# Performance work log

Hardware: AMD Instinct MI355X
Metric: run time of the kernel (lower is better)

## Reference

```python
import jax, jax.numpy as jnp
import numpy as np

DIM = 512
K = 64          # num_clusters
GHOST = 1
ALPHA = 100.0
EPS = 1e-12


def _l2norm(v, axis):
    return v / jnp.maximum(jnp.linalg.norm(v, axis=axis, keepdims=True), EPS)


def setup_inputs() -> dict:
    key = jax.random.key(0)
    k_x, k_c = jax.random.split(key)
    x = jax.random.normal(k_x, (64, DIM, 32, 32), dtype=jnp.float32)
    # centroids ~ orthogonal init in torch; random normal rows, unit-ish scale
    centroids = jax.random.normal(k_c, (K + GHOST, DIM), dtype=jnp.float32) / np.sqrt(DIM)
    conv_w = 2.0 * ALPHA * centroids            # [K+g, C] (1x1 conv kernel squeezed)
    conv_b = -ALPHA * jnp.linalg.norm(centroids, axis=1)  # [K+g]
    return {"x": x, "centroids": centroids, "conv_w": conv_w, "conv_b": conv_b}


def reference(x, centroids, conv_w, conv_b):
    N, C, H, W = x.shape
    L = H * W
    # descriptor-wise L2 normalization over channel dim
    xn = _l2norm(x, axis=1)
    xf = xn.reshape(N, C, L)                                   # [N, C, L]
    # 1x1 conv == per-location matmul; softmax over clusters
    logits = jnp.einsum('kc,ncl->nkl', conv_w, xf) + conv_b[None, :, None]
    a = jax.nn.softmax(logits, axis=1)                         # [N, K+g, L]
    # vlad[n,k,c] = sum_l a[n,k,l]*(x[n,c,l]-cent[k,c])
    #            = (a @ x^T) - (sum_l a) * cent   -- avoids NxKxCxL tensor
    weighted = jnp.einsum('nkl,ncl->nkc', a, xf)               # [N, K+g, C]
    a_sum = jnp.sum(a, axis=-1)                                # [N, K+g]
    vlad = weighted - a_sum[:, :, None] * centroids[None]      # [N, K+g, C]
    vlad = vlad[:, :K, :]                                      # drop ghost clusters
    vlad = _l2norm(vlad, axis=2)                               # intra-normalization
    vlad = vlad.reshape(N, K * C)
    vlad = _l2norm(vlad, axis=1)                               # global L2
    return vlad
```

## Files before the change

### kernel.cpp

```cpp
#include <hip/hip_runtime.h>
#include <hip/hip_bf16.h>

#define C_DIM 512
#define L_DIM 1024
#define KK 64
#define KG 65
#define KP 80

using f32x4  = __attribute__((ext_vector_type(4))) float;
using bf16x8 = __attribute__((ext_vector_type(8))) short;

union U4 { uint4 u; bf16x8 b; };

__device__ __forceinline__ unsigned bfh(float x) { return __float_as_uint(x) >> 16; }
__device__ __forceinline__ float bfh_f(float x) { return __uint_as_float(__float_as_uint(x) & 0xFFFF0000u); }

__device__ __forceinline__ unsigned pack2(float a, float b) {
    return __builtin_amdgcn_perm(__float_as_uint(b), __float_as_uint(a), 0x07060302u);
}

__global__ void k_prep(const float* __restrict__ conv_w, const float* __restrict__ conv_b,
                       unsigned short* __restrict__ wpH, unsigned short* __restrict__ wpL,
                       float* __restrict__ wb)
{
    int ch = blockIdx.x;
    int kt = blockIdx.y;
    int t  = threadIdx.x;
    for (int p = 0; p < 2; ++p) {
        int idx = p * 256 + t;
        int lane = idx >> 3, j = idx & 7;
        int k = kt * 16 + (lane & 15);
        int c = ch * 32 + (lane >> 4) * 8 + j;
        float v = (k < KG) ? conv_w[k * C_DIM + c] : 0.f;
        unsigned h = bfh(v);
        float r = v - __uint_as_float(h << 16);
        int pos = ((ch * 5 + kt) << 9) + idx;
        wpH[pos] = (unsigned short)h;
        wpL[pos] = (unsigned short)bfh(r);
    }
    if (ch == 0 && kt == 0 && t < KP) wb[t] = (t < KG) ? conv_b[t] : -1e30f;
}

__global__ __launch_bounds__(256) void k_s1(
    const float* __restrict__ x, const unsigned short* __restrict__ wpH,
    const unsigned short* __restrict__ wpL, const float* __restrict__ wb,
    unsigned* __restrict__ aPh32, unsigned* __restrict__ aPl32,
    float* __restrict__ asum_part)
{
    const int lb = blockIdx.x, n = blockIdx.y;
    const int t = threadIdx.x, lane = t & 63, w = t >> 6;
    const int arow = lane & 15;
    const int agrp = lane >> 4;
    const int lw0 = lb * 128 + w * 32;
    const int choff = (w * 4 + lb + n) & 15;

    const float* xbase = x + (size_t)n * C_DIM * L_DIM;

    f32x4 acc[5][2];
#pragma unroll
    for (int a = 0; a < 5; ++a)
#pragma unroll
        for (int b = 0; b < 2; ++b) acc[a][b] = (f32x4)0.f;
    float ss0 = 0.f, ss1 = 0.f;

    for (int ch0 = 0; ch0 < 16; ++ch0) {
        const int ch = (ch0 + choff) & 15;
        const int c0 = ch * 32;
        float e0[8], e1[8];
#pragma unroll
        for (int j = 0; j < 8; ++j) {
            float2 v = *reinterpret_cast<const float2*>(
                &xbase[(size_t)(c0 + agrp * 8 + j) * L_DIM + lw0 + 2 * arow]);
            e0[j] = v.x;
            e1[j] = v.y;
        }
#pragma unroll
        for (int j = 0; j < 8; ++j) { ss0 += e0[j] * e0[j]; ss1 += e1[j] * e1[j]; }
        U4 bh[2], bl[2];
        bh[0].u.x = pack2(e0[0], e0[1]); bh[0].u.y = pack2(e0[2], e0[3]);
        bh[0].u.z = pack2(e0[4], e0[5]); bh[0].u.w = pack2(e0[6], e0[7]);
        bh[1].u.x = pack2(e1[0], e1[1]); bh[1].u.y = pack2(e1[2], e1[3]);
        bh[1].u.z = pack2(e1[4], e1[5]); bh[1].u.w = pack2(e1[6], e1[7]);
        float r0, r1, r2, r3;
        r0 = e0[0] - bfh_f(e0[0]); r1 = e0[1] - bfh_f(e0[1]);
        r2 = e0[2] - bfh_f(e0[2]); r3 = e0[3] - bfh_f(e0[3]);
        bl[0].u.x = pack2(r0, r1); bl[0].u.y = pack2(r2, r3);
        r0 = e0[4] - bfh_f(e0[4]); r1 = e0[5] - bfh_f(e0[5]);
        r2 = e0[6] - bfh_f(e0[6]); r3 = e0[7] - bfh_f(e0[7]);
        bl[0].u.z = pack2(r0, r1); bl[0].u.w = pack2(r2, r3);
        r0 = e1[0] - bfh_f(e1[0]); r1 = e1[1] - bfh_f(e1[1]);
        r2 = e1[2] - bfh_f(e1[2]); r3 = e1[3] - bfh_f(e1[3]);
        bl[1].u.x = pack2(r0, r1); bl[1].u.y = pack2(r2, r3);
        r0 = e1[4] - bfh_f(e1[4]); r1 = e1[5] - bfh_f(e1[5]);
        r2 = e1[6] - bfh_f(e1[6]); r3 = e1[7] - bfh_f(e1[7]);
        bl[1].u.z = pack2(r0, r1); bl[1].u.w = pack2(r2, r3);
        U4 ah[5], al[5];
#pragma unroll
        for (int kt = 0; kt < 5; ++kt) {
            int poff = (((ch * 5 + kt) << 6) + lane) << 3;
            ah[kt].u = *reinterpret_cast<const uint4*>(&wpH[poff]);
            al[kt].u = *reinterpret_cast<const uint4*>(&wpL[poff]);
        }
#pragma unroll
        for (int kt = 0; kt < 5; ++kt)
#pragma unroll
            for (int lt = 0; lt < 2; ++lt) {
                acc[kt][lt] = __builtin_amdgcn_mfma_f32_16x16x32_bf16(ah[kt].b, bh[lt].b, acc[kt][lt], 0, 0, 0);
                acc[kt][lt] = __builtin_amdgcn_mfma_f32_16x16x32_bf16(ah[kt].b, bl[lt].b, acc[kt][lt], 0, 0, 0);
                acc[kt][lt] = __builtin_amdgcn_mfma_f32_16x16x32_bf16(al[kt].b, bh[lt].b, acc[kt][lt], 0, 0, 0);
            }
    }

    ss0 += __shfl_xor(ss0, 16, 64); ss0 += __shfl_xor(ss0, 32, 64);
    ss1 += __shfl_xor(ss1, 16, 64); ss1 += __shfl_xor(ss1, 32, 64);
    float invc[2];
    invc[0] = 1.0f / fmaxf(sqrtf(ss0), 1e-12f);
    invc[1] = 1.0f / fmaxf(sqrtf(ss1), 1e-12f);

    float4 wbv[5];
#pragma unroll
    for (int kt = 0; kt < 5; ++kt)
        wbv[kt] = *reinterpret_cast<const float4*>(&wb[kt * 16 + agrp * 4]);

    float aval[5][2][4];
    float rs[2];
#pragma unroll
    for (int lt = 0; lt < 2; ++lt) {
        float m = -1e30f;
#pragma unroll
        for (int kt = 0; kt < 5; ++kt)
#pragma unroll
            for (int r = 0; r < 4; ++r) {
                float lg = acc[kt][lt][r] * invc[lt] + ((const float*)&wbv[kt])[r];
                aval[kt][lt][r] = lg;
                m = fmaxf(m, lg);
            }
        m = fmaxf(m, __shfl_xor(m, 16, 64));
        m = fmaxf(m, __shfl_xor(m, 32, 64));
        float s = 0.f;
#pragma unroll
        for (int kt = 0; kt < 5; ++kt)
#pragma unroll
            for (int r = 0; r < 4; ++r) {
                float e = __expf(aval[kt][lt][r] - m);
                aval[kt][lt][r] = e;
                s += e;
            }
        s += __shfl_xor(s, 16, 64);
        s += __shfl_xor(s, 32, 64);
        rs[lt] = 1.0f / s;
    }

#pragma unroll
    for (int kt = 0; kt < 4; ++kt)
#pragma unroll
        for (int r = 0; r < 4; ++r) {
            int k = kt * 16 + agrp * 4 + r;
            float s01 = 0.f;
#pragma unroll
            for (int lt = 0; lt < 2; ++lt) {
                float a = aval[kt][lt][r] * rs[lt];
                aval[kt][lt][r] = a;
                s01 += a;
            }
#pragma unroll
            for (int off = 8; off; off >>= 1) s01 += __shfl_xor(s01, off, 64);
            if ((lane & 15) == 0)
                asum_part[((n * 8 + lb) * 4 + w) * KK + k] = s01;
            float ap0 = aval[kt][0][r] * invc[0];
            float ap1 = aval[kt][1][r] * invc[1];
            unsigned h0 = bfh(ap0), h1 = bfh(ap1);
            float q0 = ap0 - __uint_as_float(h0 << 16);
            float q1 = ap1 - __uint_as_float(h1 << 16);
            int widx = (n * KK + k) * (L_DIM / 2) + (lw0 >> 1) + arow;
            aPh32[widx] = h0 | (h1 << 16);
            aPl32[widx] = bfh(q0) | (bfh(q1) << 16);
        }
}

__global__ void k_asum(const float* __restrict__ part, float* __restrict__ a_sum)
{
    int id = blockIdx.x * 256 + threadIdx.x;
    int n = id >> 6, k = id & 63;
    float s = 0.f;
#pragma unroll
    for (int p = 0; p < 32; ++p) s += part[(n * 32 + p) * KK + k];
    a_sum[id] = s;
}

#define S2P 72
__global__ __launch_bounds__(256) void k_s2v(
    const float* __restrict__ x, const unsigned short* __restrict__ aPh,
    const unsigned short* __restrict__ aPl, const float* __restrict__ a_sum,
    const float* __restrict__ cent, float* __restrict__ vlad,
    float* __restrict__ rnpart)
{
    __shared__ unsigned short Ah[64 * S2P], Al[64 * S2P];
    __shared__ unsigned short Bh[64 * S2P], Bl[64 * S2P];
    __shared__ float rnbuf[4][64];

    const int flat = blockIdx.x;
    const int cq = flat >> 6;
    const int n  = ((flat & 7) << 3) | ((flat >> 3) & 7);
    const int t = threadIdx.x, lane = t & 63, w = t >> 6;
    const int arow = lane & 15, agrp = lane >> 4;

    f32x4 acc[4];
#pragma unroll
    for (int a = 0; a < 4; ++a) acc[a] = (f32x4)0.f;

    for (int step = 0; step < 16; ++step) {
        const int l0 = step * 64;
        __syncthreads();
#pragma unroll
        for (int p = 0; p < 2; ++p) {
            int idx = p * 256 + t;
            int k = idx >> 3;
            int lc = (idx & 7) * 8;
            size_t g = (size_t)(n * KK + k) * L_DIM + l0 + lc;
            *reinterpret_cast<uint4*>(&Ah[k * S2P + lc]) = *reinterpret_cast<const uint4*>(&aPh[g]);
            *reinterpret_cast<uint4*>(&Al[k * S2P + lc]) = *reinterpret_cast<const uint4*>(&aPl[g]);
        }
#pragma unroll
        for (int p = 0; p < 4; ++p) {
            int idx = p * 256 + t;
            int c = idx >> 4;
            int lc = (idx & 15) * 4;
            float4 v = *reinterpret_cast<const float4*>(
                &x[((size_t)n * C_DIM + cq * 64 + c) * L_DIM + l0 + lc]);
            uint2 hw, lw;
            hw.x = pack2(v.x, v.y); hw.y = pack2(v.z, v.w);
            float r0 = v.x - bfh_f(v.x), r1 = v.y - bfh_f(v.y);
            float r2 = v.z - bfh_f(v.z), r3 = v.w - bfh_f(v.w);
            lw.x = pack2(r0, r1); lw.y = pack2(r2, r3);
            *reinterpret_cast<uint2*>(&Bh[c * S2P + lc]) = hw;
            *reinterpret_cast<uint2*>(&Bl[c * S2P + lc]) = lw;
        }
        __syncthreads();
#pragma unroll
        for (int ks = 0; ks < 2; ++ks) {
            const int koff = ks * 32 + agrp * 8;
            U4 bh, bl;
            bh.u = *reinterpret_cast<const uint4*>(&Bh[(w * 16 + arow) * S2P + koff]);
            bl.u = *reinterpret_cast<const uint4*>(&Bl[(w * 16 + arow) * S2P + koff]);
#pragma unroll
            for (int kt = 0; kt < 4; ++kt) {
                U4 ah, al;
                ah.u = *reinterpret_cast<const uint4*>(&Ah[(kt * 16 + arow) * S2P + koff]);
                al.u = *reinterpret_cast<const uint4*>(&Al[(kt * 16 + arow) * S2P + koff]);
                acc[kt] = __builtin_amdgcn_mfma_f32_16x16x32_bf16(ah.b, bh.b, acc[kt], 0, 0, 0);
                acc[kt] = __builtin_amdgcn_mfma_f32_16x16x32_bf16(ah.b, bl.b, acc[kt], 0, 0, 0);
                acc[kt] = __builtin_amdgcn_mfma_f32_16x16x32_bf16(al.b, bh.b, acc[kt], 0, 0, 0);
            }
        }
    }
    const int c = cq * 64 + w * 16 + arow;
    float myrn[4][4];
#pragma unroll
    for (int kt = 0; kt < 4; ++kt)
#pragma unroll
        for (int r = 0; r < 4; ++r) {
            int k = kt * 16 + agrp * 4 + r;
            float as = a_sum[n * 64 + k];
            float cv = cent[k * C_DIM + c];
            float v = acc[kt][r] - as * cv;
            vlad[((size_t)n * KK + k) * C_DIM + c] = v;
            float sq = v * v;
            sq += __shfl_xor(sq, 1, 64);
            sq += __shfl_xor(sq, 2, 64);
            sq += __shfl_xor(sq, 4, 64);
            sq += __shfl_xor(sq, 8, 64);
            myrn[kt][r] = sq;
        }
    if (arow == 0) {
#pragma unroll
        for (int kt = 0; kt < 4; ++kt)
#pragma unroll
            for (int r = 0; r < 4; ++r)
                rnbuf[w][kt * 16 + agrp * 4 + r] = myrn[kt][r];
    }
    __syncthreads();
    if (t < 64) {
        float s = rnbuf[0][t] + rnbuf[1][t] + rnbuf[2][t] + rnbuf[3][t];
        rnpart[((size_t)n * 64 + t) * 8 + cq] = s;
    }
}

__global__ void k_scale(const float* __restrict__ rnpart, float* __restrict__ scale)
{
    int n = blockIdx.x;
    int k = threadIdx.x;
    float s = 0.f;
#pragma unroll
    for (int q = 0; q < 8; ++q) s += rnpart[((size_t)n * 64 + k) * 8 + q];
    float nrm = sqrtf(s);
    float den = fmaxf(nrm, 1e-12f);
    float tk = nrm / den;
    float tot = tk * tk;
#pragma unroll
    for (int off = 32; off; off >>= 1) tot += __shfl_down(tot, off, 64);
    tot = __shfl(tot, 0, 64);
    float g = fmaxf(sqrtf(tot), 1e-12f);
    scale[n * 64 + k] = 1.0f / (den * g);
}

__global__ void k_out(const float* __restrict__ vlad, const float* __restrict__ scale,
                      float* __restrict__ out)
{
    int nk = blockIdx.x;
    int t = threadIdx.x;
    float sc = scale[nk];
    for (int c = t; c < C_DIM; c += 256)
        out[(size_t)nk * C_DIM + c] = vlad[(size_t)nk * C_DIM + c] * sc;
}

extern "C" void kernel_launch(void* const* d_in, const int* in_sizes, int n_in,
                              void* d_out, int out_size, void* d_ws, size_t ws_size,
                              hipStream_t stream)
{
    const float* x    = (const float*)d_in[0];
    const float* cent = (const float*)d_in[1];
    const float* cw   = (const float*)d_in[2];
    const float* cb   = (const float*)d_in[3];
    float* out = (float*)d_out;
    char* ws = (char*)d_ws;

    unsigned short* wpH = (unsigned short*)(ws + 0);
    unsigned short* wpL = (unsigned short*)(ws + 131072);
    float*          wb  = (float*)(ws + 262144);
    unsigned short* aPh = (unsigned short*)(ws + 524288);
    unsigned short* aPl = (unsigned short*)(ws + 8912896);
    float* asum_part    = (float*)(ws + 17301504);
    float* a_sum        = (float*)(ws + 17825792);
    float* vlad         = (float*)(ws + 18874368);
    float* rnpart       = (float*)(ws + 27262976);
    float* scale        = (float*)(ws + 27394048);

    k_prep<<<dim3(16, 5), 256, 0, stream>>>(cw, cb, wpH, wpL, wb);
    k_s1<<<dim3(8, 64), 256, 0, stream>>>(x, wpH, wpL, wb,
                                          (unsigned*)aPh, (unsigned*)aPl, asum_part);
    k_asum<<<16, 256, 0, stream>>>(asum_part, a_sum);
    k_s2v<<<512, 256, 0, stream>>>(x, aPh, aPl, a_sum, cent, vlad, rnpart);
    k_scale<<<64, 64, 0, stream>>>(rnpart, scale);
    k_out<<<4096, 256, 0, stream>>>(vlad, scale, out);
}
```

Before: 76.82 us.

## Double-buffer x tiles through LDS with direct global-to-LDS loads in k_s1

Instead of each wave loading its x slice straight from global memory with strided float2 reads, the block now stages each 32-channel by 128-position tile into a double-buffered LDS array using global_load_lds, prefetching the next channel chunk while MFMAs run on the current one. The goal is to overlap memory latency with compute and replace scattered per-lane global reads with coalesced 16-byte loads. In exchange it adds a waitcnt and a block barrier every iteration. It also drops the per-wave channel offset, so all waves in a block now walk the channels in the same order.

```diff
diff --git a/kernel.cpp b/kernel.cpp
--- a/kernel.cpp
+++ b/kernel.cpp
@@ -17,6 +17,12 @@
 
 __device__ __forceinline__ unsigned pack2(float a, float b) {
     return __builtin_amdgcn_perm(__float_as_uint(b), __float_as_uint(a), 0x07060302u);
+}
+
+__device__ __forceinline__ void load_lds16(const void* g, void* l) {
+    __builtin_amdgcn_global_load_lds(
+        (const __attribute__((address_space(1))) void*)g,
+        (__attribute__((address_space(3))) void*)l, 16, 0, 0);
 }
 
 __global__ void k_prep(const float* __restrict__ conv_w, const float* __restrict__ conv_b,
@@ -41,20 +47,32 @@
     if (ch == 0 && kt == 0 && t < KP) wb[t] = (t < KG) ? conv_b[t] : -1e30f;
 }
 
+#define XSEG 260
 __global__ __launch_bounds__(256) void k_s1(
     const float* __restrict__ x, const unsigned short* __restrict__ wpH,
     const unsigned short* __restrict__ wpL, const float* __restrict__ wb,
     unsigned* __restrict__ aPh32, unsigned* __restrict__ aPl32,
     float* __restrict__ asum_part)
 {
+    __shared__ float xs[2][16 * XSEG];
+
     const int lb = blockIdx.x, n = blockIdx.y;
     const int t = threadIdx.x, lane = t & 63, w = t >> 6;
     const int arow = lane & 15;
     const int agrp = lane >> 4;
-    const int lw0 = lb * 128 + w * 32;
-    const int choff = (w * 4 + lb + n) & 15;
+    const int gl0 = lb * 128;
+    const int lw0 = gl0 + w * 32;
+    const int choff = (lb + n) & 15;
 
     const float* xbase = x + (size_t)n * C_DIM * L_DIM;
+
+#define STAGE(b, ch) { _Pragma("unroll") \
+    for (int i = 0; i < 4; ++i) { \
+        int s = w * 4 + i; \
+        const float* src = &xbase[(size_t)((ch) * 32 + s * 2 + (lane >> 5)) * L_DIM \
+                                  + gl0 + (lane & 31) * 4]; \
+        load_lds16(src, &xs[b][s * XSEG]); \
+    } }
 
     f32x4 acc[5][2];
 #pragma unroll
@@ -63,14 +81,21 @@
         for (int b = 0; b < 2; ++b) acc[a][b] = (f32x4)0.f;
     float ss0 = 0.f, ss1 = 0.f;
 
+    STAGE(0, choff)
+    asm volatile("s_waitcnt vmcnt(0)" ::: "memory");
+    __syncthreads();
+
+#pragma unroll 2
     for (int ch0 = 0; ch0 < 16; ++ch0) {
+        const int cur = ch0 & 1;
         const int ch = (ch0 + choff) & 15;
-        const int c0 = ch * 32;
+        if (ch0 < 15) STAGE(cur ^ 1, (ch0 + 1 + choff) & 15)
         float e0[8], e1[8];
 #pragma unroll
         for (int j = 0; j < 8; ++j) {
+            int c = agrp * 8 + j;
             float2 v = *reinterpret_cast<const float2*>(
-                &xbase[(size_t)(c0 + agrp * 8 + j) * L_DIM + lw0 + 2 * arow]);
+                &xs[cur][(c >> 1) * XSEG + (c & 1) * 128 + w * 32 + 2 * arow]);
             e0[j] = v.x;
             e1[j] = v.y;
         }
@@ -109,6 +134,8 @@
                 acc[kt][lt] = __builtin_amdgcn_mfma_f32_16x16x32_bf16(ah[kt].b, bl[lt].b, acc[kt][lt], 0, 0, 0);
                 acc[kt][lt] = __builtin_amdgcn_mfma_f32_16x16x32_bf16(al[kt].b, bh[lt].b, acc[kt][lt], 0, 0, 0);
             }
+        asm volatile("s_waitcnt vmcnt(0)" ::: "memory");
+        __syncthreads();
     }
 
     ss0 += __shfl_xor(ss0, 16, 64); ss0 += __shfl_xor(ss0, 32, 64);
```

After: 77.82 us. No clear change (+1.3%).

## Stage cluster weights into double-buffered LDS via async global-to-LDS loads in k_s1

Applied to the files above, without the earlier changes.

The bf16 hi/lo weight planes are interleaved into one buffer so each channel chunk is contiguous. Each block now copies the next chunk into a second LDS buffer with global_load_lds while it computes on the current one, and every wave reads its MFMA operands from LDS. Before, each wave loaded the weights straight from global memory. To make the shared stage possible, all waves in a block now follow the same channel order, which drops the per-wave offset. In exchange, each loop iteration adds a full vmcnt(0) wait plus a barrier, and that wait also covers the x loads.

```diff
diff --git a/kernel.cpp b/kernel.cpp
--- a/kernel.cpp
+++ b/kernel.cpp
@@ -19,9 +19,14 @@
     return __builtin_amdgcn_perm(__float_as_uint(b), __float_as_uint(a), 0x07060302u);
 }
 
+__device__ __forceinline__ void load_lds16(const void* g, void* l) {
+    __builtin_amdgcn_global_load_lds(
+        (const __attribute__((address_space(1))) void*)g,
+        (__attribute__((address_space(3))) void*)l, 16, 0, 0);
+}
+
 __global__ void k_prep(const float* __restrict__ conv_w, const float* __restrict__ conv_b,
-                       unsigned short* __restrict__ wpH, unsigned short* __restrict__ wpL,
-                       float* __restrict__ wb)
+                       unsigned short* __restrict__ wp, float* __restrict__ wb)
 {
     int ch = blockIdx.x;
     int kt = blockIdx.y;
@@ -34,27 +39,36 @@
         float v = (k < KG) ? conv_w[k * C_DIM + c] : 0.f;
         unsigned h = bfh(v);
         float r = v - __uint_as_float(h << 16);
-        int pos = ((ch * 5 + kt) << 9) + idx;
-        wpH[pos] = (unsigned short)h;
-        wpL[pos] = (unsigned short)bfh(r);
+        wp[((ch * 10 + kt) << 9) + idx]     = (unsigned short)h;
+        wp[((ch * 10 + 5 + kt) << 9) + idx] = (unsigned short)bfh(r);
     }
     if (ch == 0 && kt == 0 && t < KP) wb[t] = (t < KG) ? conv_b[t] : -1e30f;
 }
 
 __global__ __launch_bounds__(256) void k_s1(
-    const float* __restrict__ x, const unsigned short* __restrict__ wpH,
-    const unsigned short* __restrict__ wpL, const float* __restrict__ wb,
+    const float* __restrict__ x, const unsigned short* __restrict__ wp,
+    const float* __restrict__ wb,
     unsigned* __restrict__ aPh32, unsigned* __restrict__ aPl32,
     float* __restrict__ asum_part)
 {
+    __shared__ unsigned short wlds[2][10 << 9];
+
     const int lb = blockIdx.x, n = blockIdx.y;
     const int t = threadIdx.x, lane = t & 63, w = t >> 6;
     const int arow = lane & 15;
     const int agrp = lane >> 4;
     const int lw0 = lb * 128 + w * 32;
-    const int choff = (w * 4 + lb + n) & 15;
+    const int choff = (lb + n) & 15;
 
     const float* xbase = x + (size_t)n * C_DIM * L_DIM;
+
+#define WSTAGE(b, ch) { _Pragma("unroll") \
+    for (int i = 0; i < 3; ++i) { \
+        int s = w + (i << 2); \
+        if (s < 10) { \
+            const unsigned short* src = &wp[(((ch) * 10 + s) << 9) + (lane << 3)]; \
+            load_lds16(src, &wlds[b][s << 9]); \
+        } } }
 
     f32x4 acc[5][2];
 #pragma unroll
@@ -63,9 +77,16 @@
         for (int b = 0; b < 2; ++b) acc[a][b] = (f32x4)0.f;
     float ss0 = 0.f, ss1 = 0.f;
 
+    WSTAGE(0, choff)
+    asm volatile("s_waitcnt vmcnt(0)" ::: "memory");
+    __syncthreads();
+
+#pragma unroll 2
     for (int ch0 = 0; ch0 < 16; ++ch0) {
+        const int cur = ch0 & 1;
         const int ch = (ch0 + choff) & 15;
         const int c0 = ch * 32;
+        if (ch0 < 15) WSTAGE(cur ^ 1, (ch0 + 1 + choff) & 15)
         float e0[8], e1[8];
 #pragma unroll
         for (int j = 0; j < 8; ++j) {
@@ -97,9 +118,8 @@
         U4 ah[5], al[5];
 #pragma unroll
         for (int kt = 0; kt < 5; ++kt) {
-            int poff = (((ch * 5 + kt) << 6) + lane) << 3;
-            ah[kt].u = *reinterpret_cast<const uint4*>(&wpH[poff]);
-            al[kt].u = *reinterpret_cast<const uint4*>(&wpL[poff]);
+            ah[kt].u = *reinterpret_cast<const uint4*>(&wlds[cur][(kt << 9) + (lane << 3)]);
+            al[kt].u = *reinterpret_cast<const uint4*>(&wlds[cur][((5 + kt) << 9) + (lane << 3)]);
         }
 #pragma unroll
         for (int kt = 0; kt < 5; ++kt)
@@ -109,6 +129,8 @@
                 acc[kt][lt] = __builtin_amdgcn_mfma_f32_16x16x32_bf16(ah[kt].b, bl[lt].b, acc[kt][lt], 0, 0, 0);
                 acc[kt][lt] = __builtin_amdgcn_mfma_f32_16x16x32_bf16(al[kt].b, bh[lt].b, acc[kt][lt], 0, 0, 0);
             }
+        asm volatile("s_waitcnt vmcnt(0)" ::: "memory");
+        __syncthreads();
     }
 
     ss0 += __shfl_xor(ss0, 16, 64); ss0 += __shfl_xor(ss0, 32, 64);
@@ -325,8 +347,7 @@
     float* out = (float*)d_out;
     char* ws = (char*)d_ws;
 
-    unsigned short* wpH = (unsigned short*)(ws + 0);
-    unsigned short* wpL = (unsigned short*)(ws + 131072);
+    unsigned short* wp  = (unsigned short*)(ws + 0);
     float*          wb  = (float*)(ws + 262144);
     unsigned short* aPh = (unsigned short*)(ws + 524288);
     unsigned short* aPl = (unsigned short*)(ws + 8912896);
@@ -336,8 +357,8 @@
     float* rnpart       = (float*)(ws + 27262976);
     float* scale        = (float*)(ws + 27394048);
 
-    k_prep<<<dim3(16, 5), 256, 0, stream>>>(cw, cb, wpH, wpL, wb);
-    k_s1<<<dim3(8, 64), 256, 0, stream>>>(x, wpH, wpL, wb,
+    k_prep<<<dim3(16, 5), 256, 0, stream>>>(cw, cb, wp, wb);
+    k_s1<<<dim3(8, 64), 256, 0, stream>>>(x, wp, wb,
                                           (unsigned*)aPh, (unsigned*)aPl, asum_part);
     k_asum<<<16, 256, 0, stream>>>(asum_part, a_sum);
     k_s2v<<<512, 256, 0, stream>>>(x, aPh, aPl, a_sum, cent, vlad, rnpart);
```

Result: faster. 74.44 us (-3.1%).
